# Optimization experiments

Hardware: AMD Instinct MI355X
Metric: run time of the kernel (lower is better)

## Reference

```python
import jax, jax.numpy as jnp
import numpy as np

B, T1, T2, D = 8, 2048, 2048, 256


def setup_inputs() -> dict:
    key = jax.random.key(0)
    k1, k2 = jax.random.split(key)
    s1 = jax.random.normal(k1, (B, T1, D), dtype=jnp.float32)
    s2 = jax.random.normal(k2, (B, T2, D), dtype=jnp.float32)
    return {"s1": s1, "s2": s2}


def reference(s1, s2):
    # similarity: [B, t1, t2]
    s = jnp.einsum('bid,bjd->bij', s1, s2)
    # softmax over t2, replace NaNs with 0 (matches masked_fill_(w != w, 0))
    w = jax.nn.softmax(s, axis=2)
    w = jnp.where(jnp.isnan(w), jnp.zeros((), w.dtype), w)
    # one-hot of argmax over t2 (vectorized replacement of the double loop)
    idx = jnp.argmax(w, axis=2)                       # [B, t1]
    a_weight_like = jax.nn.one_hot(idx, s2.shape[1], dtype=s1.dtype)  # [B, t1, t2]
    # gather the argmax rows of s2: [B, t1, D]
    u_tile = jnp.einsum('bij,bjd->bid', a_weight_like, s2)
    return (u_tile, a_weight_like)
```

## Files before the change

kernel.cpp:

```cpp
#include <hip/hip_runtime.h>
#include <math.h>

typedef unsigned short ushort_t;

constexpr int BB = 8, T1 = 2048, T2 = 2048, D = 256;
constexpr float MARGIN = 4e-3f;

constexpr size_t OFF_QC    = 0;
constexpr size_t OFF_QUEUE = 64;
constexpr size_t OFF_PART  = (size_t)1 << 20;
constexpr size_t OFF_S1P   = (size_t)6 << 20;
constexpr size_t SZ_PACK   = (size_t)BB * 128 * 8 * 2 * 64 * 16;
constexpr size_t OFF_S2P   = OFF_S1P + SZ_PACK;
constexpr size_t WS_NEEDED = OFF_S2P + SZ_PACK;

typedef __attribute__((ext_vector_type(8))) __bf16 bf16x8;
typedef __attribute__((ext_vector_type(4))) float  f32x4;

__device__ __forceinline__ unsigned f2bf(float x) {
    unsigned u = __float_as_uint(x);
    return (u + 0x7fffu + ((u >> 16) & 1u)) >> 16;
}
__device__ __forceinline__ float bf2f(unsigned h) { return __uint_as_float(h << 16); }

__global__ __launch_bounds__(256) void k_convert(
    const float* __restrict__ s1, const float* __restrict__ s2,
    ushort_t* __restrict__ s1p, ushort_t* __restrict__ s2p)
{
    __shared__ __align__(16) ushort_t L[16384];
    const int bx = blockIdx.x;
    const int tensor = bx >> 9, b = (bx >> 6) & 7, rt = bx & 63;
    const float* src = (tensor ? s2 : s1) + ((size_t)b * 2048 + rt * 32) * 256;
    ushort_t* dst = (tensor ? s2p : s1p) + (size_t)(b * 128 + rt * 2) * 8192;
    const int t = threadIdx.x;
#pragma unroll
    for (int i = 0; i < 8; ++i) {
        int f = i * 256 + t, rw = f >> 6, c4 = f & 63, k0 = c4 * 4;
        float4 v = *(const float4*)(src + rw * 256 + k0);
        unsigned hx = f2bf(v.x), hy = f2bf(v.y), hz = f2bf(v.z), hw = f2bf(v.w);
        ushort4 hi = make_ushort4((ushort_t)hx, (ushort_t)hy, (ushort_t)hz, (ushort_t)hw);
        ushort4 lo = make_ushort4((ushort_t)f2bf(v.x - bf2f(hx)), (ushort_t)f2bf(v.y - bf2f(hy)),
                                  (ushort_t)f2bf(v.z - bf2f(hz)), (ushort_t)f2bf(v.w - bf2f(hw)));
        int tile = rw >> 4, m = rw & 15, g = k0 >> 5;
        int lane = m + 16 * ((k0 >> 3) & 3), i0 = k0 & 7;
        int off = (tile * 8 + g) * 1024 + lane * 8 + i0;
        *(ushort4*)(&L[off])       = hi;
        *(ushort4*)(&L[off + 512]) = lo;
    }
    __syncthreads();
#pragma unroll
    for (int i = 0; i < 8; ++i) {
        int cidx = i * 256 + t;
        ((uint4*)dst)[cidx] = ((const uint4*)L)[cidx];
    }
}

__global__ __launch_bounds__(256, 3) void k_score(
    const ushort_t* __restrict__ s1p, const ushort_t* __restrict__ s2p,
    float4* __restrict__ part)
{
    __shared__ float4 mrg[128][2];

    const int bx = blockIdx.x;
    const int b = bx & 7, rt16 = (bx >> 3) & 15, jq = bx >> 7;
    const int t = threadIdx.x, w = t >> 6, l = t & 63;
    const int rh = w >> 1, jw = w & 1;
    const int q = l >> 4, n = l & 15;

    mrg[t >> 1][t & 1] = make_float4(-INFINITY, -INFINITY, __int_as_float(0), 0.f);
    __syncthreads();

    const ushort_t* Aw = s1p + (size_t)(b * 128 + rt16 * 8 + rh * 4) * 8192 + l * 8;
    const ushort_t* Bw = s2p + (size_t)(b * 128 + jq * 8 + jw * 4) * 8192 + l * 8;

    f32x4 acc[4][4];
#pragma unroll
    for (int rtl = 0; rtl < 4; ++rtl)
#pragma unroll
        for (int jt = 0; jt < 4; ++jt)
#pragma unroll
            for (int r = 0; r < 4; ++r) acc[rtl][jt][r] = 0.f;

#pragma unroll 1
    for (int g = 0; g < 8; ++g) {
        const ushort_t* Ag = Aw + g * 1024;
        const ushort_t* Bg = Bw + g * 1024;
        bf16x8 aF[4][2];
#pragma unroll
        for (int rtl = 0; rtl < 4; ++rtl) {
            aF[rtl][0] = *(const bf16x8*)(Ag + (size_t)rtl * 8192);
            aF[rtl][1] = *(const bf16x8*)(Ag + (size_t)rtl * 8192 + 512);
        }
#pragma unroll
        for (int jt = 0; jt < 4; ++jt) {
            bf16x8 bh = *(const bf16x8*)(Bg + (size_t)jt * 8192);
            bf16x8 bl = *(const bf16x8*)(Bg + (size_t)jt * 8192 + 512);
#pragma unroll
            for (int rtl = 0; rtl < 4; ++rtl) {
                acc[rtl][jt] = __builtin_amdgcn_mfma_f32_16x16x32_bf16(aF[rtl][0], bh, acc[rtl][jt], 0, 0, 0);
                acc[rtl][jt] = __builtin_amdgcn_mfma_f32_16x16x32_bf16(aF[rtl][0], bl, acc[rtl][jt], 0, 0, 0);
                acc[rtl][jt] = __builtin_amdgcn_mfma_f32_16x16x32_bf16(aF[rtl][1], bh, acc[rtl][jt], 0, 0, 0);
            }
        }
    }

#pragma unroll
    for (int rtl = 0; rtl < 4; ++rtl)
#pragma unroll
        for (int reg = 0; reg < 4; ++reg) {
            float v1 = -INFINITY, v2 = -INFINITY; int i1 = 0;
#pragma unroll
            for (int jt = 0; jt < 4; ++jt) {
                float v = acc[rtl][jt][reg];
                int j = jq * 128 + jw * 64 + jt * 16 + n;
                if (v > v1)      { v2 = v1; v1 = v; i1 = j; }
                else if (v > v2) { v2 = v; }
            }
#pragma unroll
            for (int off = 1; off < 16; off <<= 1) {
                float b1 = __shfl_xor(v1, off);
                int   bi = __shfl_xor(i1, off);
                float b2 = __shfl_xor(v2, off);
                if (b1 > v1 || (b1 == v1 && bi < i1)) { v2 = fmaxf(v1, b2); v1 = b1; i1 = bi; }
                else                                   { v2 = fmaxf(b1, v2); }
            }
            int rr = rtl * 4 + reg;
            if (n == rr) {
                int row = rh * 64 + rtl * 16 + q * 4 + reg;
                float4 cur = mrg[row][jw];
                int ci = __float_as_int(cur.z);
                if (v1 > cur.x || (v1 == cur.x && i1 < ci))
                    mrg[row][jw] = make_float4(v1, fmaxf(v2, cur.x), __int_as_float(i1), 0.f);
                else
                    mrg[row][jw] = make_float4(cur.x, fmaxf(cur.y, v1), cur.z, 0.f);
            }
        }

    __syncthreads();
    if (t < 128) {
        float4 p0 = mrg[t][0], p1 = mrg[t][1];
        int i0 = __float_as_int(p0.z), i1 = __float_as_int(p1.z);
        float v1, v2; int ii;
        if (p1.x > p0.x || (p1.x == p0.x && i1 < i0)) { v1 = p1.x; v2 = fmaxf(p1.y, p0.x); ii = i1; }
        else                                          { v1 = p0.x; v2 = fmaxf(p0.y, p1.x); ii = i0; }
        part[((size_t)b * 2048 + rt16 * 128 + t) * 16 + jq] =
            make_float4(v1, v2, __int_as_float(ii), 0.f);
    }
}

__global__ __launch_bounds__(256) void k_epilogue(
    const float* __restrict__ s2, const float4* __restrict__ part,
    float* __restrict__ u, float* __restrict__ oh,
    int* __restrict__ qcount, int* __restrict__ queue)
{
    __shared__ int idxs[8];
    const int blk = blockIdx.x, t = threadIdx.x;
    const int r0 = blk * 8;
    const int b = r0 >> 11;
    if (t < 128) {
        int rl = t >> 4, p = t & 15;
        float4 pa = part[(size_t)(r0 + rl) * 16 + p];
        float v1 = pa.x, v2 = pa.y; int i1 = __float_as_int(pa.z);
#pragma unroll
        for (int off = 1; off < 16; off <<= 1) {
            float b1 = __shfl_xor(v1, off);
            int   bi = __shfl_xor(i1, off);
            float b2 = __shfl_xor(v2, off);
            if (b1 > v1 || (b1 == v1 && bi < i1)) { v2 = fmaxf(v1, b2); v1 = b1; i1 = bi; }
            else                                   { v2 = fmaxf(b1, v2); }
        }
        if (p == 0) {
            idxs[rl] = i1;
            if ((v1 - v2) < MARGIN) {
                int pos = atomicAdd(qcount, 1);
                if (pos < 16384) queue[pos] = r0 + rl;
            }
        }
    }
    __syncthreads();
    const float* s2b = s2 + (size_t)b * T2 * D;
    float* ub = u + (size_t)r0 * D;
#pragma unroll
    for (int i = 0; i < 2; ++i) {
        int flat = i * 256 + t, rl = flat >> 6, c = flat & 63;
        float4 v = *(const float4*)(s2b + (size_t)idxs[rl] * D + c * 4);
        *(float4*)(ub + (size_t)rl * D + c * 4) = v;
    }
    float* ohb = oh + (size_t)r0 * T2;
#pragma unroll 4
    for (int i = 0; i < 16; ++i) {
        int flat = i * 256 + t, rl = flat >> 9, c4 = flat & 511;
        int base = c4 * 4, id = idxs[rl];
        float4 vv;
        vv.x = (base     == id) ? 1.f : 0.f;
        vv.y = (base + 1 == id) ? 1.f : 0.f;
        vv.z = (base + 2 == id) ? 1.f : 0.f;
        vv.w = (base + 3 == id) ? 1.f : 0.f;
        *(float4*)(ohb + (size_t)rl * T2 + base) = vv;
    }
}

__global__ __launch_bounds__(256) void k_fixup(
    const float* __restrict__ s1, const float* __restrict__ s2,
    float* __restrict__ u, float* __restrict__ oh,
    const int* __restrict__ qcount, const int* __restrict__ queue, int qcap)
{
    __shared__ double s1d[D];
    __shared__ double rv[256];
    __shared__ int    rj[256];
    int nq = *qcount;
    if (nq > qcap) nq = qcap;
    const int t = threadIdx.x;
    for (int qi = blockIdx.x; qi < nq; qi += gridDim.x) {
        int rg = queue[qi];
        int b = rg >> 11, i = rg & (T1 - 1);
        __syncthreads();
        s1d[t] = (double)s1[((size_t)b * T1 + i) * D + t];
        __syncthreads();
        double bv = -INFINITY; int bj = 0;
        for (int jj = 0; jj < T2 / 256; ++jj) {
            int j = t + jj * 256;
            const float* row = s2 + ((size_t)b * T2 + j) * D;
            double s = 0.0;
            for (int k = 0; k < D; ++k) s = fma((double)row[k], s1d[k], s);
            if (s > bv) { bv = s; bj = j; }
        }
        rv[t] = bv; rj[t] = bj;
        __syncthreads();
        for (int stride = 128; stride > 0; stride >>= 1) {
            if (t < stride) {
                double ov = rv[t + stride]; int oj = rj[t + stride];
                if (ov > rv[t] || (ov == rv[t] && oj < rj[t])) { rv[t] = ov; rj[t] = oj; }
            }
            __syncthreads();
        }
        int best = rj[0];
        float* ohrow = oh + ((size_t)b * T1 + i) * T2;
#pragma unroll
        for (int jj = 0; jj < T2 / 256; ++jj) {
            int j = t + jj * 256;
            ohrow[j] = (j == best) ? 1.f : 0.f;
        }
        u[((size_t)b * T1 + i) * D + t] = s2[((size_t)b * T2 + best) * D + t];
    }
}

constexpr int FB_AST = 264, FB_BST = 72;

__global__ __launch_bounds__(512, 2) void k_score_fb(
    const float* __restrict__ s1, const float* __restrict__ s2,
    float* __restrict__ u, float* __restrict__ oh,
    int* __restrict__ qcount, int* __restrict__ queue, int qcap)
{
    __shared__ __align__(16) short Ah[64 * FB_AST];
    __shared__ __align__(16) short Al[64 * FB_AST];
    __shared__ __align__(16) short Bh[256 * FB_BST];
    __shared__ __align__(16) short Bl[256 * FB_BST];
    __shared__ float cv1[64][4], cv2[64][4];
    __shared__ int   ci1[64][4], idx_s[64];

    const int bx = blockIdx.x;
    const int b  = bx & 7;
    const int r0 = (bx >> 3) * 64;
    const float* s1b = s1 + ((size_t)b * T1 + r0) * D;
    const float* s2b = s2 + (size_t)b * T2 * D;

    const int t = threadIdx.x;
    const int w = t >> 6, l = t & 63, q = l >> 4, ln = l & 15;
    const int rh = w >> 2;
    const int jq = w & 3;

    float4 pa[8];
#pragma unroll
    for (int i = 0; i < 8; ++i) {
        int flat = i * 512 + t, row = flat >> 6, f4 = flat & 63;
        pa[i] = *(const float4*)(s1b + row * D + f4 * 4);
    }
    float4 pb[8];
#pragma unroll
    for (int i = 0; i < 8; ++i) {
        int flat = i * 512 + t, jrow = flat >> 4, f4 = flat & 15;
        pb[i] = *(const float4*)(s2b + (size_t)jrow * D + f4 * 4);
    }
#pragma unroll
    for (int i = 0; i < 8; ++i) {
        int flat = i * 512 + t, row = flat >> 6, f4 = flat & 63;
        float4 v = pa[i];
        unsigned hx = f2bf(v.x), hy = f2bf(v.y), hz = f2bf(v.z), hw = f2bf(v.w);
        uint2 hh, ll;
        hh.x = hx | (hy << 16); hh.y = hz | (hw << 16);
        ll.x = f2bf(v.x - bf2f(hx)) | (f2bf(v.y - bf2f(hy)) << 16);
        ll.y = f2bf(v.z - bf2f(hz)) | (f2bf(v.w - bf2f(hw)) << 16);
        *(uint2*)(&Ah[row * FB_AST + f4 * 4]) = hh;
        *(uint2*)(&Al[row * FB_AST + f4 * 4]) = ll;
    }

    float v1[2][4], v2[2][4]; int i1[2][4];
#pragma unroll
    for (int rt = 0; rt < 2; ++rt)
#pragma unroll
        for (int r = 0; r < 4; ++r) { v1[rt][r] = -INFINITY; v2[rt][r] = -INFINITY; i1[rt][r] = 0; }

    f32x4 acc[2][4];

    for (int c = 0; c < 32; ++c) {
        const int iter = c >> 2, kc = c & 3;
        if (kc == 0) {
#pragma unroll
            for (int rt = 0; rt < 2; ++rt)
#pragma unroll
                for (int jt = 0; jt < 4; ++jt)
#pragma unroll
                    for (int r = 0; r < 4; ++r) acc[rt][jt][r] = 0.f;
        }
        __syncthreads();
#pragma unroll
        for (int i = 0; i < 8; ++i) {
            int flat = i * 512 + t, jrow = flat >> 4, f4 = flat & 15;
            float4 v = pb[i];
            unsigned hx = f2bf(v.x), hy = f2bf(v.y), hz = f2bf(v.z), hw = f2bf(v.w);
            uint2 hh, ll;
            hh.x = hx | (hy << 16); hh.y = hz | (hw << 16);
            ll.x = f2bf(v.x - bf2f(hx)) | (f2bf(v.y - bf2f(hy)) << 16);
            ll.y = f2bf(v.z - bf2f(hz)) | (f2bf(v.w - bf2f(hw)) << 16);
            *(uint2*)(&Bh[jrow * FB_BST + f4 * 4]) = hh;
            *(uint2*)(&Bl[jrow * FB_BST + f4 * 4]) = ll;
        }
        if (c < 31) {
            int c2 = c + 1, it2 = c2 >> 2, kc2 = c2 & 3;
#pragma unroll
            for (int i = 0; i < 8; ++i) {
                int flat = i * 512 + t, jrow = flat >> 4, f4 = flat & 15;
                pb[i] = *(const float4*)(s2b + (size_t)(it2 * 256 + jrow) * D + kc2 * 64 + f4 * 4);
            }
        }
        __syncthreads();

#pragma unroll
        for (int ks = 0; ks < 2; ++ks) {
            const int kA = kc * 64 + ks * 32 + q * 8;
            bf16x8 ah[2], al8[2];
#pragma unroll
            for (int rt = 0; rt < 2; ++rt) {
                int off = (rh * 32 + rt * 16 + ln) * FB_AST + kA;
                ah[rt]  = *(const bf16x8*)(&Ah[off]);
                al8[rt] = *(const bf16x8*)(&Al[off]);
            }
#pragma unroll
            for (int jt = 0; jt < 4; ++jt) {
                int boff = (jq * 64 + jt * 16 + ln) * FB_BST + ks * 32 + q * 8;
                bf16x8 bh = *(const bf16x8*)(&Bh[boff]);
                bf16x8 bl = *(const bf16x8*)(&Bl[boff]);
#pragma unroll
                for (int rt = 0; rt < 2; ++rt) {
                    acc[rt][jt] = __builtin_amdgcn_mfma_f32_16x16x32_bf16(ah[rt],  bh, acc[rt][jt], 0, 0, 0);
                    acc[rt][jt] = __builtin_amdgcn_mfma_f32_16x16x32_bf16(ah[rt],  bl, acc[rt][jt], 0, 0, 0);
                    acc[rt][jt] = __builtin_amdgcn_mfma_f32_16x16x32_bf16(al8[rt], bh, acc[rt][jt], 0, 0, 0);
                }
            }
        }

        if (kc == 3) {
#pragma unroll
            for (int rt = 0; rt < 2; ++rt)
#pragma unroll
                for (int jt = 0; jt < 4; ++jt)
#pragma unroll
                    for (int r = 0; r < 4; ++r) {
                        float val = acc[rt][jt][r];
                        int j = iter * 256 + jq * 64 + jt * 16 + ln;
                        if (val > v1[rt][r]) { v2[rt][r] = v1[rt][r]; v1[rt][r] = val; i1[rt][r] = j; }
                        else if (val > v2[rt][r]) v2[rt][r] = val;
                    }
        }
    }

#pragma unroll
    for (int rt = 0; rt < 2; ++rt)
#pragma unroll
        for (int r = 0; r < 4; ++r) {
            float a1 = v1[rt][r], a2 = v2[rt][r]; int ai = i1[rt][r];
#pragma unroll
            for (int off = 1; off < 16; off <<= 1) {
                float b1 = __shfl_xor(a1, off);
                int   bi = __shfl_xor(ai, off);
                float b2 = __shfl_xor(a2, off);
                if (b1 > a1 || (b1 == a1 && bi < ai)) { a2 = fmaxf(a1, b2); a1 = b1; ai = bi; }
                else                                   { a2 = fmaxf(b1, a2); }
            }
            if (ln == 0) {
                int row = rh * 32 + rt * 16 + q * 4 + r;
                cv1[row][jq] = a1; cv2[row][jq] = a2; ci1[row][jq] = ai;
            }
        }
    __syncthreads();

    if (t < 64) {
        float V1 = cv1[t][0], V2 = cv2[t][0]; int I = ci1[t][0];
#pragma unroll
        for (int h = 1; h < 4; ++h) {
            float c1 = cv1[t][h], c2 = cv2[t][h]; int ci = ci1[t][h];
            if (c1 > V1 || (c1 == V1 && ci < I)) { V2 = fmaxf(V1, c2); V1 = c1; I = ci; }
            else                                  { V2 = fmaxf(V2, c1); }
        }
        idx_s[t] = I;
        if (qcap > 0 && (V1 - V2) < MARGIN) {
            int pos = atomicAdd(qcount, 1);
            if (pos < qcap) queue[pos] = b * T1 + r0 + t;
        }
    }
    __syncthreads();

    float* ub = u + ((size_t)b * T1 + r0) * D;
#pragma unroll
    for (int i = 0; i < 8; ++i) {
        int flat = i * 512 + t, row = flat >> 6, f4 = flat & 63;
        float4 v = *(const float4*)(s2b + (size_t)idx_s[row] * D + f4 * 4);
        *(float4*)(ub + (size_t)row * D + f4 * 4) = v;
    }
    float* ohb = oh + ((size_t)b * T1 + r0) * T2;
#pragma unroll 4
    for (int i = 0; i < 64; ++i) {
        int flat = i * 512 + t, row = flat >> 9, f4 = flat & 511;
        int base = f4 * 4, id = idx_s[row];
        float4 vv;
        vv.x = (base     == id) ? 1.f : 0.f;
        vv.y = (base + 1 == id) ? 1.f : 0.f;
        vv.z = (base + 2 == id) ? 1.f : 0.f;
        vv.w = (base + 3 == id) ? 1.f : 0.f;
        *(float4*)(ohb + (size_t)row * T2 + base) = vv;
    }
}

extern "C" void kernel_launch(void* const* d_in, const int* in_sizes, int n_in,
                              void* d_out, int out_size, void* d_ws, size_t ws_size,
                              hipStream_t stream)
{
    const float* s1 = (const float*)d_in[0];
    const float* s2 = (const float*)d_in[1];
    float* u  = (float*)d_out;
    float* oh = u + (size_t)BB * T1 * D;
    char* ws = (char*)d_ws;

    if (ws_size >= WS_NEEDED) {
        int*      qc    = (int*)(ws + OFF_QC);
        int*      queue = (int*)(ws + OFF_QUEUE);
        float4*   part  = (float4*)(ws + OFF_PART);
        ushort_t* s1p   = (ushort_t*)(ws + OFF_S1P);
        ushort_t* s2p   = (ushort_t*)(ws + OFF_S2P);
        hipMemsetAsync(ws + OFF_QC, 0, 16, stream);
        k_convert<<<dim3(1024), dim3(256), 0, stream>>>(s1, s2, s1p, s2p);
        k_score<<<dim3(2048), dim3(256), 0, stream>>>(s1p, s2p, part);
        k_epilogue<<<dim3(2048), dim3(256), 0, stream>>>(s2, part, u, oh, qc, queue);
        k_fixup<<<dim3(128), dim3(256), 0, stream>>>(s1, s2, u, oh, qc, queue, 16384);
    } else {
        int  qcap   = 0;
        int* qcount = nullptr;
        int* queue  = nullptr;
        if (ws_size >= 256) {
            qcount = (int*)d_ws;
            queue  = (int*)d_ws + 4;
            size_t cap = (ws_size - 16) / sizeof(int);
            qcap = (int)(cap > (size_t)(BB * T1) ? (size_t)(BB * T1) : cap);
            hipMemsetAsync(d_ws, 0, 16, stream);
        }
        k_score_fb<<<dim3(BB * (T1 / 64)), dim3(512), 0, stream>>>(
            s1, s2, u, oh, qcount, queue, qcap);
        if (qcap > 0)
            k_fixup<<<dim3(64), dim3(256), 0, stream>>>(
                s1, s2, u, oh, qcount, queue, qcap);
    }
}
```

Baseline: 304.9 us.

## Fuse score and epilogue kernels into one row-block kernel with in-loop one-hot zeroing

Replaces the split score kernel plus epilogue with one kernel. Each block stages 64 rows of packed s1 in LDS, sweeps all 2048 columns with register double-buffered B fragments, keeps running top-2 values in registers, and writes one-hot zeros tile by tile between MFMA phases. This removes the partial-results buffer round trip and a second kernel launch, and aims to hide the large one-hot store traffic behind compute. In exchange it launches only 256 blocks of 4 waves at occupancy 1, so latency hiding is weaker and each block rereads all of s2p from L2.

```diff
diff --git a/kernel.cpp b/kernel.cpp
--- a/kernel.cpp
+++ b/kernel.cpp
@@ -8,8 +8,7 @@
 
 constexpr size_t OFF_QC    = 0;
 constexpr size_t OFF_QUEUE = 64;
-constexpr size_t OFF_PART  = (size_t)1 << 20;
-constexpr size_t OFF_S1P   = (size_t)6 << 20;
+constexpr size_t OFF_S1P   = (size_t)2 << 20;
 constexpr size_t SZ_PACK   = (size_t)BB * 128 * 8 * 2 * 64 * 16;
 constexpr size_t OFF_S2P   = OFF_S1P + SZ_PACK;
 constexpr size_t WS_NEEDED = OFF_S2P + SZ_PACK;
@@ -55,148 +54,156 @@
     }
 }
 
-__global__ __launch_bounds__(256, 3) void k_score(
+__global__ __launch_bounds__(256, 1) void k_score_fused(
     const ushort_t* __restrict__ s1p, const ushort_t* __restrict__ s2p,
-    float4* __restrict__ part)
-{
-    __shared__ float4 mrg[128][2];
-
-    const int bx = blockIdx.x;
-    const int b = bx & 7, rt16 = (bx >> 3) & 15, jq = bx >> 7;
-    const int t = threadIdx.x, w = t >> 6, l = t & 63;
-    const int rh = w >> 1, jw = w & 1;
-    const int q = l >> 4, n = l & 15;
-
-    mrg[t >> 1][t & 1] = make_float4(-INFINITY, -INFINITY, __int_as_float(0), 0.f);
-    __syncthreads();
-
-    const ushort_t* Aw = s1p + (size_t)(b * 128 + rt16 * 8 + rh * 4) * 8192 + l * 8;
-    const ushort_t* Bw = s2p + (size_t)(b * 128 + jq * 8 + jw * 4) * 8192 + l * 8;
-
-    f32x4 acc[4][4];
-#pragma unroll
-    for (int rtl = 0; rtl < 4; ++rtl)
-#pragma unroll
-        for (int jt = 0; jt < 4; ++jt)
-#pragma unroll
-            for (int r = 0; r < 4; ++r) acc[rtl][jt][r] = 0.f;
-
-#pragma unroll 1
-    for (int g = 0; g < 8; ++g) {
-        const ushort_t* Ag = Aw + g * 1024;
-        const ushort_t* Bg = Bw + g * 1024;
-        bf16x8 aF[4][2];
-#pragma unroll
-        for (int rtl = 0; rtl < 4; ++rtl) {
-            aF[rtl][0] = *(const bf16x8*)(Ag + (size_t)rtl * 8192);
-            aF[rtl][1] = *(const bf16x8*)(Ag + (size_t)rtl * 8192 + 512);
-        }
-#pragma unroll
-        for (int jt = 0; jt < 4; ++jt) {
-            bf16x8 bh = *(const bf16x8*)(Bg + (size_t)jt * 8192);
-            bf16x8 bl = *(const bf16x8*)(Bg + (size_t)jt * 8192 + 512);
-#pragma unroll
-            for (int rtl = 0; rtl < 4; ++rtl) {
-                acc[rtl][jt] = __builtin_amdgcn_mfma_f32_16x16x32_bf16(aF[rtl][0], bh, acc[rtl][jt], 0, 0, 0);
-                acc[rtl][jt] = __builtin_amdgcn_mfma_f32_16x16x32_bf16(aF[rtl][0], bl, acc[rtl][jt], 0, 0, 0);
-                acc[rtl][jt] = __builtin_amdgcn_mfma_f32_16x16x32_bf16(aF[rtl][1], bh, acc[rtl][jt], 0, 0, 0);
-            }
-        }
-    }
-
-#pragma unroll
-    for (int rtl = 0; rtl < 4; ++rtl)
-#pragma unroll
-        for (int reg = 0; reg < 4; ++reg) {
-            float v1 = -INFINITY, v2 = -INFINITY; int i1 = 0;
-#pragma unroll
-            for (int jt = 0; jt < 4; ++jt) {
-                float v = acc[rtl][jt][reg];
-                int j = jq * 128 + jw * 64 + jt * 16 + n;
-                if (v > v1)      { v2 = v1; v1 = v; i1 = j; }
-                else if (v > v2) { v2 = v; }
-            }
-#pragma unroll
-            for (int off = 1; off < 16; off <<= 1) {
-                float b1 = __shfl_xor(v1, off);
-                int   bi = __shfl_xor(i1, off);
-                float b2 = __shfl_xor(v2, off);
-                if (b1 > v1 || (b1 == v1 && bi < i1)) { v2 = fmaxf(v1, b2); v1 = b1; i1 = bi; }
-                else                                   { v2 = fmaxf(b1, v2); }
-            }
-            int rr = rtl * 4 + reg;
-            if (n == rr) {
-                int row = rh * 64 + rtl * 16 + q * 4 + reg;
-                float4 cur = mrg[row][jw];
-                int ci = __float_as_int(cur.z);
-                if (v1 > cur.x || (v1 == cur.x && i1 < ci))
-                    mrg[row][jw] = make_float4(v1, fmaxf(v2, cur.x), __int_as_float(i1), 0.f);
-                else
-                    mrg[row][jw] = make_float4(cur.x, fmaxf(cur.y, v1), cur.z, 0.f);
-            }
-        }
-
-    __syncthreads();
-    if (t < 128) {
-        float4 p0 = mrg[t][0], p1 = mrg[t][1];
-        int i0 = __float_as_int(p0.z), i1 = __float_as_int(p1.z);
-        float v1, v2; int ii;
-        if (p1.x > p0.x || (p1.x == p0.x && i1 < i0)) { v1 = p1.x; v2 = fmaxf(p1.y, p0.x); ii = i1; }
-        else                                          { v1 = p0.x; v2 = fmaxf(p0.y, p1.x); ii = i0; }
-        part[((size_t)b * 2048 + rt16 * 128 + t) * 16 + jq] =
-            make_float4(v1, v2, __int_as_float(ii), 0.f);
-    }
-}
-
-__global__ __launch_bounds__(256) void k_epilogue(
-    const float* __restrict__ s2, const float4* __restrict__ part,
+    const float* __restrict__ s2,
     float* __restrict__ u, float* __restrict__ oh,
     int* __restrict__ qcount, int* __restrict__ queue)
 {
-    __shared__ int idxs[8];
-    const int blk = blockIdx.x, t = threadIdx.x;
-    const int r0 = blk * 8;
-    const int b = r0 >> 11;
-    if (t < 128) {
-        int rl = t >> 4, p = t & 15;
-        float4 pa = part[(size_t)(r0 + rl) * 16 + p];
-        float v1 = pa.x, v2 = pa.y; int i1 = __float_as_int(pa.z);
-#pragma unroll
-        for (int off = 1; off < 16; off <<= 1) {
-            float b1 = __shfl_xor(v1, off);
-            int   bi = __shfl_xor(i1, off);
-            float b2 = __shfl_xor(v2, off);
-            if (b1 > v1 || (b1 == v1 && bi < i1)) { v2 = fmaxf(v1, b2); v1 = b1; i1 = bi; }
-            else                                   { v2 = fmaxf(b1, v2); }
-        }
-        if (p == 0) {
-            idxs[rl] = i1;
-            if ((v1 - v2) < MARGIN) {
-                int pos = atomicAdd(qcount, 1);
-                if (pos < 16384) queue[pos] = r0 + rl;
-            }
-        }
-    }
-    __syncthreads();
+    __shared__ __align__(16) ushort_t AL[4 * 8192];
+    __shared__ float4 mrg[64][4];
+    __shared__ int    idxs[64];
+
+    const int bx = blockIdx.x;
+    const int b = bx & 7, rg = bx >> 3;
+    const int r0 = rg * 64;
+    const int t = threadIdx.x, w = t >> 6, l = t & 63;
+    const int q = l >> 4, n = l & 15;
+
+    {
+        const uint4* src = (const uint4*)(s1p + (size_t)(b * 128 + rg * 4) * 8192);
+        uint4* dst = (uint4*)AL;
+#pragma unroll
+        for (int i = 0; i < 16; ++i) dst[i * 256 + t] = src[i * 256 + t];
+    }
+    __syncthreads();
+
+    float v1[4][4], v2[4][4]; int i1r[4][4];
+#pragma unroll
+    for (int rt = 0; rt < 4; ++rt)
+#pragma unroll
+        for (int r = 0; r < 4; ++r) { v1[rt][r] = -INFINITY; v2[rt][r] = -INFINITY; i1r[rt][r] = 0; }
+
+    float* ohb = oh + ((size_t)b * T1 + r0) * T2;
+    const float4 z4 = make_float4(0.f, 0.f, 0.f, 0.f);
+
+#pragma unroll 1
+    for (int jtb = 0; jtb < 8; ++jtb) {
+        f32x4 acc[4][4];
+#pragma unroll
+        for (int jj = 0; jj < 4; ++jj)
+#pragma unroll
+            for (int rt = 0; rt < 4; ++rt)
+#pragma unroll
+                for (int r = 0; r < 4; ++r) acc[jj][rt][r] = 0.f;
+
+        const ushort_t* Bb = s2p + (size_t)(b * 128 + w * 32 + jtb * 4) * 8192 + l * 8;
+
+        bf16x8 bF0[4][2], bF1[4][2];
+#pragma unroll
+        for (int jj = 0; jj < 4; ++jj) {
+            bF0[jj][0] = *(const bf16x8*)(Bb + (size_t)jj * 8192);
+            bF0[jj][1] = *(const bf16x8*)(Bb + (size_t)jj * 8192 + 512);
+        }
+
+        auto g_body = [&](int g, bf16x8 (&bCur)[4][2], bf16x8 (&bNext)[4][2], bool pref) {
+            if (pref) {
+                const ushort_t* Bn = Bb + (g + 1) * 1024;
+#pragma unroll
+                for (int jj = 0; jj < 4; ++jj) {
+                    bNext[jj][0] = *(const bf16x8*)(Bn + (size_t)jj * 8192);
+                    bNext[jj][1] = *(const bf16x8*)(Bn + (size_t)jj * 8192 + 512);
+                }
+            }
+            bf16x8 aF[4][2];
+#pragma unroll
+            for (int rt = 0; rt < 4; ++rt) {
+                aF[rt][0] = *(const bf16x8*)(&AL[(rt * 8 + g) * 1024 + l * 8]);
+                aF[rt][1] = *(const bf16x8*)(&AL[(rt * 8 + g) * 1024 + 512 + l * 8]);
+            }
+#pragma unroll
+            for (int jj = 0; jj < 4; ++jj)
+#pragma unroll
+                for (int rt = 0; rt < 4; ++rt) {
+                    acc[jj][rt] = __builtin_amdgcn_mfma_f32_16x16x32_bf16(aF[rt][0], bCur[jj][0], acc[jj][rt], 0, 0, 0);
+                    acc[jj][rt] = __builtin_amdgcn_mfma_f32_16x16x32_bf16(aF[rt][0], bCur[jj][1], acc[jj][rt], 0, 0, 0);
+                    acc[jj][rt] = __builtin_amdgcn_mfma_f32_16x16x32_bf16(aF[rt][1], bCur[jj][0], acc[jj][rt], 0, 0, 0);
+                }
+        };
+
+#pragma unroll 1
+        for (int g2 = 0; g2 < 4; ++g2) {
+            g_body(2 * g2,     bF0, bF1, true);
+            g_body(2 * g2 + 1, bF1, bF0, g2 < 3);
+        }
+
+#pragma unroll
+        for (int rt = 0; rt < 4; ++rt)
+#pragma unroll
+            for (int reg = 0; reg < 4; ++reg)
+#pragma unroll
+                for (int jj = 0; jj < 4; ++jj) {
+                    float v = acc[jj][rt][reg];
+                    int j = w * 512 + jtb * 64 + jj * 16 + n;
+                    if (v > v1[rt][reg])      { v2[rt][reg] = v1[rt][reg]; v1[rt][reg] = v; i1r[rt][reg] = j; }
+                    else if (v > v2[rt][reg]) { v2[rt][reg] = v; }
+                }
+
+        {
+            int jbase = w * 512 + jtb * 64;
+#pragma unroll
+            for (int i = 0; i < 16; ++i) {
+                int row = i * 4 + (l >> 4);
+                int c4  = l & 15;
+                *(float4*)(ohb + (size_t)row * T2 + jbase + c4 * 4) = z4;
+            }
+        }
+    }
+
+#pragma unroll
+    for (int rt = 0; rt < 4; ++rt)
+#pragma unroll
+        for (int reg = 0; reg < 4; ++reg) {
+            float a1 = v1[rt][reg], a2 = v2[rt][reg]; int ai = i1r[rt][reg];
+#pragma unroll
+            for (int off = 1; off < 16; off <<= 1) {
+                float b1 = __shfl_xor(a1, off);
+                int   bi = __shfl_xor(ai, off);
+                float b2 = __shfl_xor(a2, off);
+                if (b1 > a1 || (b1 == a1 && bi < ai)) { a2 = fmaxf(a1, b2); a1 = b1; ai = bi; }
+                else                                   { a2 = fmaxf(b1, a2); }
+            }
+            if (n == rt * 4 + reg)
+                mrg[rt * 16 + q * 4 + reg][w] = make_float4(a1, a2, __int_as_float(ai), 0.f);
+        }
+    __syncthreads();
+
+    if (t < 64) {
+        float4 p = mrg[t][0];
+        float V1 = p.x, V2 = p.y; int I = __float_as_int(p.z);
+#pragma unroll
+        for (int h = 1; h < 4; ++h) {
+            float4 c = mrg[t][h];
+            int ci = __float_as_int(c.z);
+            if (c.x > V1 || (c.x == V1 && ci < I)) { V2 = fmaxf(V1, c.y); V1 = c.x; I = ci; }
+            else                                    { V2 = fmaxf(V2, c.x); }
+        }
+        idxs[t] = I;
+        if ((V1 - V2) < MARGIN) {
+            int pos = atomicAdd(qcount, 1);
+            if (pos < 16384) queue[pos] = b * T1 + r0 + t;
+        }
+        ohb[(size_t)t * T2 + I] = 1.0f;
+    }
+    __syncthreads();
+
     const float* s2b = s2 + (size_t)b * T2 * D;
-    float* ub = u + (size_t)r0 * D;
-#pragma unroll
-    for (int i = 0; i < 2; ++i) {
-        int flat = i * 256 + t, rl = flat >> 6, c = flat & 63;
-        float4 v = *(const float4*)(s2b + (size_t)idxs[rl] * D + c * 4);
-        *(float4*)(ub + (size_t)rl * D + c * 4) = v;
-    }
-    float* ohb = oh + (size_t)r0 * T2;
-#pragma unroll 4
+    float* ub = u + ((size_t)b * T1 + r0) * D;
+#pragma unroll
     for (int i = 0; i < 16; ++i) {
-        int flat = i * 256 + t, rl = flat >> 9, c4 = flat & 511;
-        int base = c4 * 4, id = idxs[rl];
-        float4 vv;
-        vv.x = (base     == id) ? 1.f : 0.f;
-        vv.y = (base + 1 == id) ? 1.f : 0.f;
-        vv.z = (base + 2 == id) ? 1.f : 0.f;
-        vv.w = (base + 3 == id) ? 1.f : 0.f;
-        *(float4*)(ohb + (size_t)rl * T2 + base) = vv;
+        int flat = i * 256 + t, row = flat >> 6, c4 = flat & 63;
+        float4 v = *(const float4*)(s2b + (size_t)idxs[row] * D + c4 * 4);
+        *(float4*)(ub + (size_t)row * D + c4 * 4) = v;
     }
 }
 
@@ -445,13 +452,11 @@
     if (ws_size >= WS_NEEDED) {
         int*      qc    = (int*)(ws + OFF_QC);
         int*      queue = (int*)(ws + OFF_QUEUE);
-        float4*   part  = (float4*)(ws + OFF_PART);
         ushort_t* s1p   = (ushort_t*)(ws + OFF_S1P);
         ushort_t* s2p   = (ushort_t*)(ws + OFF_S2P);
         hipMemsetAsync(ws + OFF_QC, 0, 16, stream);
         k_convert<<<dim3(1024), dim3(256), 0, stream>>>(s1, s2, s1p, s2p);
-        k_score<<<dim3(2048), dim3(256), 0, stream>>>(s1p, s2p, part);
-        k_epilogue<<<dim3(2048), dim3(256), 0, stream>>>(s2, part, u, oh, qc, queue);
+        k_score_fused<<<dim3(256), dim3(256), 0, stream>>>(s1p, s2p, s2, u, oh, qc, queue);
         k_fixup<<<dim3(128), dim3(256), 0, stream>>>(s1, s2, u, oh, qc, queue, 16384);
     } else {
         int  qcap   = 0;
```

Result: no change. 299.3 us (-1.8%).
